# Kernel tuning notes

Hardware: AMD Instinct MI355X
Metric: run time of the kernel (lower is better)

Reference implementation:

```python
import jax, jax.numpy as jnp
import numpy as np

VOXEL_RES = 4
CLASSES = 40


def setup_inputs() -> dict:
    key = jax.random.key(0)
    kx, kw, kb = jax.random.split(key, 3)
    B, N = 64, 100000
    x = jax.random.normal(kx, (B, N, 3), dtype=jnp.float32)
    F = VOXEL_RES ** 3
    bound = 1.0 / np.sqrt(F)  # torch Linear default init range
    W = jax.random.uniform(kw, (CLASSES, F), minval=-bound, maxval=bound, dtype=jnp.float32)
    b = jax.random.uniform(kb, (CLASSES,), minval=-bound, maxval=bound, dtype=jnp.float32)
    return {"x": x, "W": W, "b": b}


def reference(x, W, b):
    # x: (B, N, 3). Faithful to torch.histogramdd(bins=R): the histogram range
    # per dimension is [min, max] of the data; the last bin is right-inclusive.
    B, N, _ = x.shape
    R = VOXEL_RES
    mn = jnp.min(x, axis=1, keepdims=True)  # (B, 1, 3)
    mx = jnp.max(x, axis=1, keepdims=True)  # (B, 1, 3)
    # bin index = floor((v - min) / (max - min) * R), clipped so v == max -> R-1
    idx = jnp.floor((x - mn) / (mx - mn) * R).astype(jnp.int32)
    idx = jnp.clip(idx, 0, R - 1)  # (B, N, 3)
    flat = idx[..., 0] * R * R + idx[..., 1] * R + idx[..., 2]  # (B, N)
    flat = flat + (jnp.arange(B, dtype=jnp.int32) * (R ** 3))[:, None]
    counts = jax.ops.segment_sum(
        jnp.ones((B * N,), dtype=x.dtype), flat.reshape(-1), num_segments=B * R ** 3
    ).reshape(B, R ** 3)
    counts = counts / N  # fraction of points per voxel
    class_outputs = counts @ W.T + b  # (B, classes)
    return class_outputs
```

## Files before the change

kernel.cpp:

```cpp
#include <hip/hip_runtime.h>

#define VR 4
#define NVOX 64
#define NCLS 40
#define NB 64
#define NPTS 100000
#define BPB 16
#define G_PER_B (NPTS / 4)
#define F4_PER_B (NPTS * 3 / 4)
#define STRIDE_G (BPB * 256)
#define FLT_BIG 3.402823466e38f

__global__ __launch_bounds__(256) void minmax_k(const float4* __restrict__ x,
                                                float* __restrict__ pmin,
                                                float* __restrict__ pmax) {
    const int b = blockIdx.x / BPB;
    const int sub = blockIdx.x % BPB;
    const float4* xb = x + (size_t)b * F4_PER_B;

    float mn0 = FLT_BIG, mn1 = FLT_BIG, mn2 = FLT_BIG;
    float mx0 = -FLT_BIG, mx1 = -FLT_BIG, mx2 = -FLT_BIG;

    for (int base = sub * 256; base < G_PER_B; base += STRIDE_G) {
        int g = base + (int)threadIdx.x;
        bool valid = g < G_PER_B;
        int gc = valid ? g : (G_PER_B - 1);
        float4 a = xb[3 * gc];
        float4 c = xb[3 * gc + 1];
        float4 e = xb[3 * gc + 2];
        if (valid) {
            mn0 = fminf(mn0, fminf(fminf(a.x, a.w), fminf(c.z, e.y)));
            mx0 = fmaxf(mx0, fmaxf(fmaxf(a.x, a.w), fmaxf(c.z, e.y)));
            mn1 = fminf(mn1, fminf(fminf(a.y, c.x), fminf(c.w, e.z)));
            mx1 = fmaxf(mx1, fmaxf(fmaxf(a.y, c.x), fmaxf(c.w, e.z)));
            mn2 = fminf(mn2, fminf(fminf(a.z, c.y), fminf(e.x, e.w)));
            mx2 = fmaxf(mx2, fmaxf(fmaxf(a.z, c.y), fmaxf(e.x, e.w)));
        }
    }

    #pragma unroll
    for (int off = 32; off > 0; off >>= 1) {
        mn0 = fminf(mn0, __shfl_down(mn0, off, 64));
        mn1 = fminf(mn1, __shfl_down(mn1, off, 64));
        mn2 = fminf(mn2, __shfl_down(mn2, off, 64));
        mx0 = fmaxf(mx0, __shfl_down(mx0, off, 64));
        mx1 = fmaxf(mx1, __shfl_down(mx1, off, 64));
        mx2 = fmaxf(mx2, __shfl_down(mx2, off, 64));
    }

    __shared__ float smn[4][3], smx[4][3];
    const int lane = threadIdx.x & 63;
    const int wv = threadIdx.x >> 6;
    if (lane == 0) {
        smn[wv][0] = mn0; smn[wv][1] = mn1; smn[wv][2] = mn2;
        smx[wv][0] = mx0; smx[wv][1] = mx1; smx[wv][2] = mx2;
    }
    __syncthreads();
    if (threadIdx.x < 3) {
        const int d = threadIdx.x;
        float a = smn[0][d], z = smx[0][d];
        #pragma unroll
        for (int w = 1; w < 4; w++) {
            a = fminf(a, smn[w][d]);
            z = fmaxf(z, smx[w][d]);
        }
        pmin[(b * BPB + sub) * 3 + d] = a;
        pmax[(b * BPB + sub) * 3 + d] = z;
    }
}

__device__ __forceinline__ int bin1(float v, float mn, float s4) {
    int i = (int)((v - mn) * s4);
    return i > (VR - 1) ? (VR - 1) : i;
}

__device__ __forceinline__ void tally(int v, unsigned long long vm,
                                      const unsigned long long* ns,
                                      unsigned& cnt) {
    unsigned long long b0 = __ballot(v & 1);
    unsigned long long b1 = __ballot(v & 2);
    unsigned long long b2 = __ballot(v & 4);
    unsigned long long b3 = __ballot(v & 8);
    unsigned long long b4 = __ballot(v & 16);
    unsigned long long b5 = __ballot(v & 32);
    unsigned long long m = vm & (b0 ^ ns[0]) & (b1 ^ ns[1]) & (b2 ^ ns[2])
                              & (b3 ^ ns[3]) & (b4 ^ ns[4]) & (b5 ^ ns[5]);
    cnt += (unsigned)__popcll(m);
}

__global__ __launch_bounds__(256) void hist_k(const float4* __restrict__ x,
                                              const float* __restrict__ pmin,
                                              const float* __restrict__ pmax,
                                              unsigned* __restrict__ phist) {
    const int b = blockIdx.x / BPB;
    const int sub = blockIdx.x % BPB;
    const float4* xb = x + (size_t)b * F4_PER_B;
    const int lane = threadIdx.x & 63;
    const int wv = threadIdx.x >> 6;

    __shared__ float smm[6];
    if (threadIdx.x < 6) {
        int d = threadIdx.x % 3;
        bool isMax = threadIdx.x >= 3;
        float r = isMax ? -FLT_BIG : FLT_BIG;
        for (int s = 0; s < BPB; s++) {
            float v = isMax ? pmax[(b * BPB + s) * 3 + d]
                            : pmin[(b * BPB + s) * 3 + d];
            r = isMax ? fmaxf(r, v) : fminf(r, v);
        }
        smm[threadIdx.x] = r;
    }
    __syncthreads();
    const float mn_0 = smm[0], mn_1 = smm[1], mn_2 = smm[2];
    const float s4_0 = (float)VR / (smm[3] - smm[0]);
    const float s4_1 = (float)VR / (smm[4] - smm[1]);
    const float s4_2 = (float)VR / (smm[5] - smm[2]);

    unsigned long long ns[6];
    #pragma unroll
    for (int k = 0; k < 6; k++)
        ns[k] = ((lane >> k) & 1) ? 0ull : ~0ull;

    unsigned cnt = 0;
    for (int base = sub * 256; base < G_PER_B; base += STRIDE_G) {
        int g = base + (int)threadIdx.x;
        bool valid = g < G_PER_B;
        int gc = valid ? g : (G_PER_B - 1);
        float4 a = xb[3 * gc];
        float4 c = xb[3 * gc + 1];
        float4 e = xb[3 * gc + 2];
        unsigned long long vm = __ballot(valid);
        int v0 = bin1(a.x, mn_0, s4_0) * 16 + bin1(a.y, mn_1, s4_1) * 4 + bin1(a.z, mn_2, s4_2);
        int v1 = bin1(a.w, mn_0, s4_0) * 16 + bin1(c.x, mn_1, s4_1) * 4 + bin1(c.y, mn_2, s4_2);
        int v2 = bin1(c.z, mn_0, s4_0) * 16 + bin1(c.w, mn_1, s4_1) * 4 + bin1(e.x, mn_2, s4_2);
        int v3 = bin1(e.y, mn_0, s4_0) * 16 + bin1(e.z, mn_1, s4_1) * 4 + bin1(e.w, mn_2, s4_2);
        tally(v0, vm, ns, cnt);
        tally(v1, vm, ns, cnt);
        tally(v2, vm, ns, cnt);
        tally(v3, vm, ns, cnt);
    }

    __shared__ unsigned swh[4][NVOX];
    swh[wv][lane] = cnt;
    __syncthreads();
    if (threadIdx.x < NVOX) {
        phist[(b * BPB + sub) * NVOX + threadIdx.x] =
            swh[0][threadIdx.x] + swh[1][threadIdx.x] +
            swh[2][threadIdx.x] + swh[3][threadIdx.x];
    }
}

__global__ __launch_bounds__(256) void gemv_k(const unsigned* __restrict__ phist,
                                              const float* __restrict__ W,
                                              const float* __restrict__ bias,
                                              float* __restrict__ out) {
    const int b = blockIdx.x;
    __shared__ float fh[NVOX];
    __shared__ float sW[NCLS * NVOX];

    if (threadIdx.x < NVOX) {
        unsigned s = 0;
        for (int p = 0; p < BPB; p++)
            s += phist[(b * BPB + p) * NVOX + threadIdx.x];
        fh[threadIdx.x] = (float)s * (1.0f / (float)NPTS);
    }
    for (int i = threadIdx.x; i < NCLS * NVOX; i += 256)
        sW[i] = W[i];
    __syncthreads();

    if (threadIdx.x < NCLS) {
        const int c = threadIdx.x;
        float acc = 0.f;
        #pragma unroll
        for (int f = 0; f < NVOX; f++)
            acc += fh[f] * sW[c * NVOX + f];
        out[b * NCLS + c] = acc + bias[c];
    }
}

extern "C" void kernel_launch(void* const* d_in, const int* in_sizes, int n_in,
                              void* d_out, int out_size, void* d_ws, size_t ws_size,
                              hipStream_t stream) {
    const float* x = (const float*)d_in[0];
    const float* W = (const float*)d_in[1];
    const float* bias = (const float*)d_in[2];
    float* out = (float*)d_out;

    float* pmin = (float*)d_ws;
    float* pmax = pmin + NB * BPB * 3;
    unsigned* phist = (unsigned*)(pmax + NB * BPB * 3);

    minmax_k<<<NB * BPB, 256, 0, stream>>>((const float4*)x, pmin, pmax);
    hist_k<<<NB * BPB, 256, 0, stream>>>((const float4*)x, pmin, pmax, phist);
    gemv_k<<<NB, 256, 0, stream>>>(phist, W, bias, out);
}
```

Before: 125.8 us.

## Fuse minmax, histogram and GEMV into one cooperative kernel with grid syncs

Merges the three kernel launches into a single cooperative kernel that uses grid-wide syncs between the min/max reduction, the histogram pass and the final GEMV. The aim is to remove launch overhead and inter-kernel gaps. Because each block handles the same data slice in both passes, its portion of x may still be in L2 or MALL when the histogram pass rereads it. The cost is two grid barriers. The grid of 1024 blocks must also be co-resident for the cooperative launch to succeed, or the launch fails.

```diff
diff --git a/kernel.cpp b/kernel.cpp
--- a/kernel.cpp
+++ b/kernel.cpp
@@ -1,4 +1,7 @@
 #include <hip/hip_runtime.h>
+#include <hip/hip_cooperative_groups.h>
+
+namespace cg = cooperative_groups;
 
 #define VR 4
 #define NVOX 64
@@ -6,68 +9,11 @@
 #define NB 64
 #define NPTS 100000
 #define BPB 16
+#define GRID (NB * BPB)
 #define G_PER_B (NPTS / 4)
 #define F4_PER_B (NPTS * 3 / 4)
 #define STRIDE_G (BPB * 256)
 #define FLT_BIG 3.402823466e38f
-
-__global__ __launch_bounds__(256) void minmax_k(const float4* __restrict__ x,
-                                                float* __restrict__ pmin,
-                                                float* __restrict__ pmax) {
-    const int b = blockIdx.x / BPB;
-    const int sub = blockIdx.x % BPB;
-    const float4* xb = x + (size_t)b * F4_PER_B;
-
-    float mn0 = FLT_BIG, mn1 = FLT_BIG, mn2 = FLT_BIG;
-    float mx0 = -FLT_BIG, mx1 = -FLT_BIG, mx2 = -FLT_BIG;
-
-    for (int base = sub * 256; base < G_PER_B; base += STRIDE_G) {
-        int g = base + (int)threadIdx.x;
-        bool valid = g < G_PER_B;
-        int gc = valid ? g : (G_PER_B - 1);
-        float4 a = xb[3 * gc];
-        float4 c = xb[3 * gc + 1];
-        float4 e = xb[3 * gc + 2];
-        if (valid) {
-            mn0 = fminf(mn0, fminf(fminf(a.x, a.w), fminf(c.z, e.y)));
-            mx0 = fmaxf(mx0, fmaxf(fmaxf(a.x, a.w), fmaxf(c.z, e.y)));
-            mn1 = fminf(mn1, fminf(fminf(a.y, c.x), fminf(c.w, e.z)));
-            mx1 = fmaxf(mx1, fmaxf(fmaxf(a.y, c.x), fmaxf(c.w, e.z)));
-            mn2 = fminf(mn2, fminf(fminf(a.z, c.y), fminf(e.x, e.w)));
-            mx2 = fmaxf(mx2, fmaxf(fmaxf(a.z, c.y), fmaxf(e.x, e.w)));
-        }
-    }
-
-    #pragma unroll
-    for (int off = 32; off > 0; off >>= 1) {
-        mn0 = fminf(mn0, __shfl_down(mn0, off, 64));
-        mn1 = fminf(mn1, __shfl_down(mn1, off, 64));
-        mn2 = fminf(mn2, __shfl_down(mn2, off, 64));
-        mx0 = fmaxf(mx0, __shfl_down(mx0, off, 64));
-        mx1 = fmaxf(mx1, __shfl_down(mx1, off, 64));
-        mx2 = fmaxf(mx2, __shfl_down(mx2, off, 64));
-    }
-
-    __shared__ float smn[4][3], smx[4][3];
-    const int lane = threadIdx.x & 63;
-    const int wv = threadIdx.x >> 6;
-    if (lane == 0) {
-        smn[wv][0] = mn0; smn[wv][1] = mn1; smn[wv][2] = mn2;
-        smx[wv][0] = mx0; smx[wv][1] = mx1; smx[wv][2] = mx2;
-    }
-    __syncthreads();
-    if (threadIdx.x < 3) {
-        const int d = threadIdx.x;
-        float a = smn[0][d], z = smx[0][d];
-        #pragma unroll
-        for (int w = 1; w < 4; w++) {
-            a = fminf(a, smn[w][d]);
-            z = fmaxf(z, smx[w][d]);
-        }
-        pmin[(b * BPB + sub) * 3 + d] = a;
-        pmax[(b * BPB + sub) * 3 + d] = z;
-    }
-}
 
 __device__ __forceinline__ int bin1(float v, float mn, float s4) {
     int i = (int)((v - mn) * s4);
@@ -88,100 +34,159 @@
     cnt += (unsigned)__popcll(m);
 }
 
-__global__ __launch_bounds__(256) void hist_k(const float4* __restrict__ x,
-                                              const float* __restrict__ pmin,
-                                              const float* __restrict__ pmax,
-                                              unsigned* __restrict__ phist) {
+__global__ __launch_bounds__(256) void fused_k(const float4* __restrict__ x,
+                                               float* __restrict__ pmin,
+                                               float* __restrict__ pmax,
+                                               unsigned* __restrict__ phist,
+                                               const float* __restrict__ W,
+                                               const float* __restrict__ bias,
+                                               float* __restrict__ out) {
+    cg::grid_group grid = cg::this_grid();
     const int b = blockIdx.x / BPB;
     const int sub = blockIdx.x % BPB;
     const float4* xb = x + (size_t)b * F4_PER_B;
     const int lane = threadIdx.x & 63;
     const int wv = threadIdx.x >> 6;
 
-    __shared__ float smm[6];
-    if (threadIdx.x < 6) {
-        int d = threadIdx.x % 3;
-        bool isMax = threadIdx.x >= 3;
-        float r = isMax ? -FLT_BIG : FLT_BIG;
-        for (int s = 0; s < BPB; s++) {
-            float v = isMax ? pmax[(b * BPB + s) * 3 + d]
-                            : pmin[(b * BPB + s) * 3 + d];
-            r = isMax ? fmaxf(r, v) : fminf(r, v);
-        }
-        smm[threadIdx.x] = r;
+    {
+        float mn0 = FLT_BIG, mn1 = FLT_BIG, mn2 = FLT_BIG;
+        float mx0 = -FLT_BIG, mx1 = -FLT_BIG, mx2 = -FLT_BIG;
+
+        for (int base = sub * 256; base < G_PER_B; base += STRIDE_G) {
+            int g = base + (int)threadIdx.x;
+            bool valid = g < G_PER_B;
+            int gc = valid ? g : (G_PER_B - 1);
+            float4 a = xb[3 * gc];
+            float4 c = xb[3 * gc + 1];
+            float4 e = xb[3 * gc + 2];
+            if (valid) {
+                mn0 = fminf(mn0, fminf(fminf(a.x, a.w), fminf(c.z, e.y)));
+                mx0 = fmaxf(mx0, fmaxf(fmaxf(a.x, a.w), fmaxf(c.z, e.y)));
+                mn1 = fminf(mn1, fminf(fminf(a.y, c.x), fminf(c.w, e.z)));
+                mx1 = fmaxf(mx1, fmaxf(fmaxf(a.y, c.x), fmaxf(c.w, e.z)));
+                mn2 = fminf(mn2, fminf(fminf(a.z, c.y), fminf(e.x, e.w)));
+                mx2 = fmaxf(mx2, fmaxf(fmaxf(a.z, c.y), fmaxf(e.x, e.w)));
+            }
+        }
+
+        #pragma unroll
+        for (int off = 32; off > 0; off >>= 1) {
+            mn0 = fminf(mn0, __shfl_down(mn0, off, 64));
+            mn1 = fminf(mn1, __shfl_down(mn1, off, 64));
+            mn2 = fminf(mn2, __shfl_down(mn2, off, 64));
+            mx0 = fmaxf(mx0, __shfl_down(mx0, off, 64));
+            mx1 = fmaxf(mx1, __shfl_down(mx1, off, 64));
+            mx2 = fmaxf(mx2, __shfl_down(mx2, off, 64));
+        }
+
+        __shared__ float smn[4][3], smx[4][3];
+        if (lane == 0) {
+            smn[wv][0] = mn0; smn[wv][1] = mn1; smn[wv][2] = mn2;
+            smx[wv][0] = mx0; smx[wv][1] = mx1; smx[wv][2] = mx2;
+        }
+        __syncthreads();
+        if (threadIdx.x < 3) {
+            const int d = threadIdx.x;
+            float a = smn[0][d], z = smx[0][d];
+            #pragma unroll
+            for (int w = 1; w < 4; w++) {
+                a = fminf(a, smn[w][d]);
+                z = fmaxf(z, smx[w][d]);
+            }
+            pmin[(b * BPB + sub) * 3 + d] = a;
+            pmax[(b * BPB + sub) * 3 + d] = z;
+        }
     }
-    __syncthreads();
-    const float mn_0 = smm[0], mn_1 = smm[1], mn_2 = smm[2];
-    const float s4_0 = (float)VR / (smm[3] - smm[0]);
-    const float s4_1 = (float)VR / (smm[4] - smm[1]);
-    const float s4_2 = (float)VR / (smm[5] - smm[2]);
-
-    unsigned long long ns[6];
-    #pragma unroll
-    for (int k = 0; k < 6; k++)
-        ns[k] = ((lane >> k) & 1) ? 0ull : ~0ull;
-
-    unsigned cnt = 0;
-    for (int base = sub * 256; base < G_PER_B; base += STRIDE_G) {
-        int g = base + (int)threadIdx.x;
-        bool valid = g < G_PER_B;
-        int gc = valid ? g : (G_PER_B - 1);
-        float4 a = xb[3 * gc];
-        float4 c = xb[3 * gc + 1];
-        float4 e = xb[3 * gc + 2];
-        unsigned long long vm = __ballot(valid);
-        int v0 = bin1(a.x, mn_0, s4_0) * 16 + bin1(a.y, mn_1, s4_1) * 4 + bin1(a.z, mn_2, s4_2);
-        int v1 = bin1(a.w, mn_0, s4_0) * 16 + bin1(c.x, mn_1, s4_1) * 4 + bin1(c.y, mn_2, s4_2);
-        int v2 = bin1(c.z, mn_0, s4_0) * 16 + bin1(c.w, mn_1, s4_1) * 4 + bin1(e.x, mn_2, s4_2);
-        int v3 = bin1(e.y, mn_0, s4_0) * 16 + bin1(e.z, mn_1, s4_1) * 4 + bin1(e.w, mn_2, s4_2);
-        tally(v0, vm, ns, cnt);
-        tally(v1, vm, ns, cnt);
-        tally(v2, vm, ns, cnt);
-        tally(v3, vm, ns, cnt);
+
+    __threadfence();
+    grid.sync();
+
+    {
+        __shared__ float smm[6];
+        if (threadIdx.x < 6) {
+            int d = threadIdx.x % 3;
+            bool isMax = threadIdx.x >= 3;
+            float r = isMax ? -FLT_BIG : FLT_BIG;
+            for (int s = 0; s < BPB; s++) {
+                float v = isMax ? pmax[(b * BPB + s) * 3 + d]
+                                : pmin[(b * BPB + s) * 3 + d];
+                r = isMax ? fmaxf(r, v) : fminf(r, v);
+            }
+            smm[threadIdx.x] = r;
+        }
+        __syncthreads();
+        const float mn_0 = smm[0], mn_1 = smm[1], mn_2 = smm[2];
+        const float s4_0 = (float)VR / (smm[3] - smm[0]);
+        const float s4_1 = (float)VR / (smm[4] - smm[1]);
+        const float s4_2 = (float)VR / (smm[5] - smm[2]);
+
+        unsigned long long ns[6];
+        #pragma unroll
+        for (int k = 0; k < 6; k++)
+            ns[k] = ((lane >> k) & 1) ? 0ull : ~0ull;
+
+        unsigned cnt = 0;
+        for (int base = sub * 256; base < G_PER_B; base += STRIDE_G) {
+            int g = base + (int)threadIdx.x;
+            bool valid = g < G_PER_B;
+            int gc = valid ? g : (G_PER_B - 1);
+            float4 a = xb[3 * gc];
+            float4 c = xb[3 * gc + 1];
+            float4 e = xb[3 * gc + 2];
+            unsigned long long vm = __ballot(valid);
+            int v0 = bin1(a.x, mn_0, s4_0) * 16 + bin1(a.y, mn_1, s4_1) * 4 + bin1(a.z, mn_2, s4_2);
+            int v1 = bin1(a.w, mn_0, s4_0) * 16 + bin1(c.x, mn_1, s4_1) * 4 + bin1(c.y, mn_2, s4_2);
+            int v2 = bin1(c.z, mn_0, s4_0) * 16 + bin1(c.w, mn_1, s4_1) * 4 + bin1(e.x, mn_2, s4_2);
+            int v3 = bin1(e.y, mn_0, s4_0) * 16 + bin1(e.z, mn_1, s4_1) * 4 + bin1(e.w, mn_2, s4_2);
+            tally(v0, vm, ns, cnt);
+            tally(v1, vm, ns, cnt);
+            tally(v2, vm, ns, cnt);
+            tally(v3, vm, ns, cnt);
+        }
+
+        __shared__ unsigned swh[4][NVOX];
+        swh[wv][lane] = cnt;
+        __syncthreads();
+        if (threadIdx.x < NVOX) {
+            phist[(b * BPB + sub) * NVOX + threadIdx.x] =
+                swh[0][threadIdx.x] + swh[1][threadIdx.x] +
+                swh[2][threadIdx.x] + swh[3][threadIdx.x];
+        }
     }
 
-    __shared__ unsigned swh[4][NVOX];
-    swh[wv][lane] = cnt;
-    __syncthreads();
-    if (threadIdx.x < NVOX) {
-        phist[(b * BPB + sub) * NVOX + threadIdx.x] =
-            swh[0][threadIdx.x] + swh[1][threadIdx.x] +
-            swh[2][threadIdx.x] + swh[3][threadIdx.x];
-    }
-}
-
-__global__ __launch_bounds__(256) void gemv_k(const unsigned* __restrict__ phist,
-                                              const float* __restrict__ W,
-                                              const float* __restrict__ bias,
-                                              float* __restrict__ out) {
-    const int b = blockIdx.x;
-    __shared__ float fh[NVOX];
-    __shared__ float sW[NCLS * NVOX];
-
-    if (threadIdx.x < NVOX) {
-        unsigned s = 0;
-        for (int p = 0; p < BPB; p++)
-            s += phist[(b * BPB + p) * NVOX + threadIdx.x];
-        fh[threadIdx.x] = (float)s * (1.0f / (float)NPTS);
-    }
-    for (int i = threadIdx.x; i < NCLS * NVOX; i += 256)
-        sW[i] = W[i];
-    __syncthreads();
-
-    if (threadIdx.x < NCLS) {
-        const int c = threadIdx.x;
-        float acc = 0.f;
-        #pragma unroll
-        for (int f = 0; f < NVOX; f++)
-            acc += fh[f] * sW[c * NVOX + f];
-        out[b * NCLS + c] = acc + bias[c];
+    __threadfence();
+    grid.sync();
+
+    if (blockIdx.x < NB) {
+        const int bb = blockIdx.x;
+        __shared__ float fh[NVOX];
+        __shared__ float sW[NCLS * NVOX];
+
+        if (threadIdx.x < NVOX) {
+            unsigned s = 0;
+            for (int p = 0; p < BPB; p++)
+                s += phist[(bb * BPB + p) * NVOX + threadIdx.x];
+            fh[threadIdx.x] = (float)s * (1.0f / (float)NPTS);
+        }
+        for (int i = threadIdx.x; i < NCLS * NVOX; i += 256)
+            sW[i] = W[i];
+        __syncthreads();
+
+        if (threadIdx.x < NCLS) {
+            const int c = threadIdx.x;
+            float acc = 0.f;
+            #pragma unroll
+            for (int f = 0; f < NVOX; f++)
+                acc += fh[f] * sW[c * NVOX + f];
+            out[bb * NCLS + c] = acc + bias[c];
+        }
     }
 }
 
 extern "C" void kernel_launch(void* const* d_in, const int* in_sizes, int n_in,
                               void* d_out, int out_size, void* d_ws, size_t ws_size,
                               hipStream_t stream) {
-    const float* x = (const float*)d_in[0];
+    const float4* x = (const float4*)d_in[0];
     const float* W = (const float*)d_in[1];
     const float* bias = (const float*)d_in[2];
     float* out = (float*)d_out;
@@ -190,7 +195,8 @@
     float* pmax = pmin + NB * BPB * 3;
     unsigned* phist = (unsigned*)(pmax + NB * BPB * 3);
 
-    minmax_k<<<NB * BPB, 256, 0, stream>>>((const float4*)x, pmin, pmax);
-    hist_k<<<NB * BPB, 256, 0, stream>>>((const float4*)x, pmin, pmax, phist);
-    gemv_k<<<NB, 256, 0, stream>>>(phist, W, bias, out);
-}
+    void* args[] = {(void*)&x, (void*)&pmin, (void*)&pmax, (void*)&phist,
+                    (void*)&W, (void*)&bias, (void*)&out};
+    hipLaunchCooperativeKernel((void*)fused_k, dim3(GRID), dim3(256), args, 0,
+                               stream);
+}
```

Measured after the change: 473.0 us. +276.0%, slower.

## Use exact contiguous chunking with all loads issued up front per block

Applied to the files above, without the earlier changes.

Each batch is now split into 25 blocks of exactly 1000 point-groups. Each thread loads its four groups (12 float4s) into registers at the start, so the strided loop with bounds checks is gone. The hist kernel also issues its point loads before the global min/max reduction, hiding that latency, and does the reduction with wave shuffles instead of a serial loop. The cost is 6 idle lanes per block and higher register use from the 12 buffered float4s.

```diff
diff --git a/kernel.cpp b/kernel.cpp
--- a/kernel.cpp
+++ b/kernel.cpp
@@ -5,10 +5,11 @@
 #define NCLS 40
 #define NB 64
 #define NPTS 100000
-#define BPB 16
+#define BPB 25
+#define GPB 1000
+#define ATH 250
 #define G_PER_B (NPTS / 4)
 #define F4_PER_B (NPTS * 3 / 4)
-#define STRIDE_G (BPB * 256)
 #define FLT_BIG 3.402823466e38f
 
 __global__ __launch_bounds__(256) void minmax_k(const float4* __restrict__ x,
@@ -17,18 +18,26 @@
     const int b = blockIdx.x / BPB;
     const int sub = blockIdx.x % BPB;
     const float4* xb = x + (size_t)b * F4_PER_B;
+    const int tid = threadIdx.x;
+    const int lane = tid & 63;
+    const int wv = tid >> 6;
+    const int t = tid < ATH ? tid : ATH - 1;
+
+    float4 d[12];
+    #pragma unroll
+    for (int k = 0; k < 4; ++k) {
+        int g = sub * GPB + k * ATH + t;
+        d[3 * k + 0] = xb[3 * g + 0];
+        d[3 * k + 1] = xb[3 * g + 1];
+        d[3 * k + 2] = xb[3 * g + 2];
+    }
 
     float mn0 = FLT_BIG, mn1 = FLT_BIG, mn2 = FLT_BIG;
     float mx0 = -FLT_BIG, mx1 = -FLT_BIG, mx2 = -FLT_BIG;
-
-    for (int base = sub * 256; base < G_PER_B; base += STRIDE_G) {
-        int g = base + (int)threadIdx.x;
-        bool valid = g < G_PER_B;
-        int gc = valid ? g : (G_PER_B - 1);
-        float4 a = xb[3 * gc];
-        float4 c = xb[3 * gc + 1];
-        float4 e = xb[3 * gc + 2];
-        if (valid) {
+    if (tid < ATH) {
+        #pragma unroll
+        for (int k = 0; k < 4; ++k) {
+            float4 a = d[3 * k], c = d[3 * k + 1], e = d[3 * k + 2];
             mn0 = fminf(mn0, fminf(fminf(a.x, a.w), fminf(c.z, e.y)));
             mx0 = fmaxf(mx0, fmaxf(fmaxf(a.x, a.w), fmaxf(c.z, e.y)));
             mn1 = fminf(mn1, fminf(fminf(a.y, c.x), fminf(c.w, e.z)));
@@ -49,23 +58,21 @@
     }
 
     __shared__ float smn[4][3], smx[4][3];
-    const int lane = threadIdx.x & 63;
-    const int wv = threadIdx.x >> 6;
     if (lane == 0) {
         smn[wv][0] = mn0; smn[wv][1] = mn1; smn[wv][2] = mn2;
         smx[wv][0] = mx0; smx[wv][1] = mx1; smx[wv][2] = mx2;
     }
     __syncthreads();
-    if (threadIdx.x < 3) {
-        const int d = threadIdx.x;
-        float a = smn[0][d], z = smx[0][d];
+    if (tid < 3) {
+        const int dd = tid;
+        float a = smn[0][dd], z = smx[0][dd];
         #pragma unroll
         for (int w = 1; w < 4; w++) {
-            a = fminf(a, smn[w][d]);
-            z = fmaxf(z, smx[w][d]);
-        }
-        pmin[(b * BPB + sub) * 3 + d] = a;
-        pmax[(b * BPB + sub) * 3 + d] = z;
+            a = fminf(a, smn[w][dd]);
+            z = fmaxf(z, smx[w][dd]);
+        }
+        pmin[(b * BPB + sub) * 3 + dd] = a;
+        pmax[(b * BPB + sub) * 3 + dd] = z;
     }
 }
 
@@ -95,58 +102,78 @@
     const int b = blockIdx.x / BPB;
     const int sub = blockIdx.x % BPB;
     const float4* xb = x + (size_t)b * F4_PER_B;
-    const int lane = threadIdx.x & 63;
-    const int wv = threadIdx.x >> 6;
+    const int tid = threadIdx.x;
+    const int lane = tid & 63;
+    const int wv = tid >> 6;
+    const int t = tid < ATH ? tid : ATH - 1;
+
+    float4 d[12];
+    #pragma unroll
+    for (int k = 0; k < 4; ++k) {
+        int g = sub * GPB + k * ATH + t;
+        d[3 * k + 0] = xb[3 * g + 0];
+        d[3 * k + 1] = xb[3 * g + 1];
+        d[3 * k + 2] = xb[3 * g + 2];
+    }
 
     __shared__ float smm[6];
-    if (threadIdx.x < 6) {
-        int d = threadIdx.x % 3;
-        bool isMax = threadIdx.x >= 3;
-        float r = isMax ? -FLT_BIG : FLT_BIG;
-        for (int s = 0; s < BPB; s++) {
-            float v = isMax ? pmax[(b * BPB + s) * 3 + d]
-                            : pmin[(b * BPB + s) * 3 + d];
-            r = isMax ? fmaxf(r, v) : fminf(r, v);
-        }
-        smm[threadIdx.x] = r;
+    if (wv < 2) {
+        const float* src = (wv == 0) ? pmin : pmax;
+        float v0, v1, v2;
+        if (lane < BPB) {
+            v0 = src[(b * BPB + lane) * 3 + 0];
+            v1 = src[(b * BPB + lane) * 3 + 1];
+            v2 = src[(b * BPB + lane) * 3 + 2];
+        } else {
+            v0 = v1 = v2 = (wv == 0) ? FLT_BIG : -FLT_BIG;
+        }
+        #pragma unroll
+        for (int off = 16; off > 0; off >>= 1) {
+            float u0 = __shfl_down(v0, off, 64);
+            float u1 = __shfl_down(v1, off, 64);
+            float u2 = __shfl_down(v2, off, 64);
+            if (wv == 0) {
+                v0 = fminf(v0, u0); v1 = fminf(v1, u1); v2 = fminf(v2, u2);
+            } else {
+                v0 = fmaxf(v0, u0); v1 = fmaxf(v1, u1); v2 = fmaxf(v2, u2);
+            }
+        }
+        if (lane == 0) {
+            smm[wv * 3 + 0] = v0; smm[wv * 3 + 1] = v1; smm[wv * 3 + 2] = v2;
+        }
     }
     __syncthreads();
     const float mn_0 = smm[0], mn_1 = smm[1], mn_2 = smm[2];
-    const float s4_0 = (float)VR / (smm[3] - smm[0]);
-    const float s4_1 = (float)VR / (smm[4] - smm[1]);
-    const float s4_2 = (float)VR / (smm[5] - smm[2]);
+    const float s4_0 = (float)VR / (smm[3] - mn_0);
+    const float s4_1 = (float)VR / (smm[4] - mn_1);
+    const float s4_2 = (float)VR / (smm[5] - mn_2);
 
     unsigned long long ns[6];
     #pragma unroll
     for (int k = 0; k < 6; k++)
         ns[k] = ((lane >> k) & 1) ? 0ull : ~0ull;
-
-    unsigned cnt = 0;
-    for (int base = sub * 256; base < G_PER_B; base += STRIDE_G) {
-        int g = base + (int)threadIdx.x;
-        bool valid = g < G_PER_B;
-        int gc = valid ? g : (G_PER_B - 1);
-        float4 a = xb[3 * gc];
-        float4 c = xb[3 * gc + 1];
-        float4 e = xb[3 * gc + 2];
-        unsigned long long vm = __ballot(valid);
+    const unsigned long long vm = __ballot(tid < ATH);
+
+    unsigned c_ = 0;
+    #pragma unroll
+    for (int k = 0; k < 4; ++k) {
+        float4 a = d[3 * k], c = d[3 * k + 1], e = d[3 * k + 2];
         int v0 = bin1(a.x, mn_0, s4_0) * 16 + bin1(a.y, mn_1, s4_1) * 4 + bin1(a.z, mn_2, s4_2);
         int v1 = bin1(a.w, mn_0, s4_0) * 16 + bin1(c.x, mn_1, s4_1) * 4 + bin1(c.y, mn_2, s4_2);
         int v2 = bin1(c.z, mn_0, s4_0) * 16 + bin1(c.w, mn_1, s4_1) * 4 + bin1(e.x, mn_2, s4_2);
         int v3 = bin1(e.y, mn_0, s4_0) * 16 + bin1(e.z, mn_1, s4_1) * 4 + bin1(e.w, mn_2, s4_2);
-        tally(v0, vm, ns, cnt);
-        tally(v1, vm, ns, cnt);
-        tally(v2, vm, ns, cnt);
-        tally(v3, vm, ns, cnt);
+        tally(v0, vm, ns, c_);
+        tally(v1, vm, ns, c_);
+        tally(v2, vm, ns, c_);
+        tally(v3, vm, ns, c_);
     }
 
     __shared__ unsigned swh[4][NVOX];
-    swh[wv][lane] = cnt;
-    __syncthreads();
-    if (threadIdx.x < NVOX) {
-        phist[(b * BPB + sub) * NVOX + threadIdx.x] =
-            swh[0][threadIdx.x] + swh[1][threadIdx.x] +
-            swh[2][threadIdx.x] + swh[3][threadIdx.x];
+    swh[wv][lane] = c_;
+    __syncthreads();
+    if (tid < NVOX) {
+        phist[(b * BPB + sub) * NVOX + tid] =
+            swh[0][tid] + swh[1][tid] + swh[2][tid] + swh[3][tid];
     }
 }
 
```

Result: slower. 131.2 us (+4.3%).
